# Kernel tuning notes

Hardware: AMD Instinct MI355X
Metric: run time of the kernel (lower is better)

Reference implementation:

```python
import jax, jax.numpy as jnp
import numpy as np

PAD = 20
MAX_DISP = 20
STRIDE2 = 2


def setup_inputs() -> dict:
    key = jax.random.key(0)
    k1, k2 = jax.random.split(key)
    B, C, H, W = 8, 256, 96, 128
    input1 = jax.random.normal(k1, (B, C, H, W), dtype=jnp.float32)
    input2 = jax.random.normal(k2, (B, C, H, W), dtype=jnp.float32)
    return {"input1": input1, "input2": input2}


def reference(input1, input2):
    B, C, H, W = input1.shape
    # zero-pad f2 spatially by PAD on all sides, as ZeroPad2d(pad_size)
    f2pad = jnp.pad(input2, ((0, 0), (0, 0), (PAD, PAD), (PAD, PAD)))
    # displacement offsets: range(i, i + 2*max_disp + 1, stride2) -> 21 per axis
    offs = jnp.arange(0, 2 * MAX_DISP + 1, STRIDE2)
    dy, dx = jnp.meshgrid(offs, offs, indexing="ij")  # h-major flatten matches torch flatten(-2,-1)
    dydx = jnp.stack([dy.ravel(), dx.ravel()], axis=-1)  # [441, 2]

    def step(_, d):
        # shifted view of f2pad: window element (dy, dx) for every pixel (i, j)
        win = jax.lax.dynamic_slice(f2pad, (0, 0, d[0], d[1]), (B, C, H, W))
        # per-pixel inner product over channels
        return None, jnp.einsum("bchw,bchw->bhw", input1, win)

    _, out = jax.lax.scan(step, None, dydx)  # [441, B, H, W]
    out = jnp.transpose(out, (1, 0, 2, 3))  # [B, 441, H, W]
    return out / C
```

## Files before the change

kernel.cpp:

```cpp
#include <hip/hip_runtime.h>
#include <hip/hip_bf16.h>


#define NB 8
#define NC 256
#define NH 96
#define NW 128
#define NU 64
#define ND 21
#define NK 441
#define HW (NH * NW)
#define ROWDW 8192
#define NR 97

typedef __attribute__((ext_vector_type(8))) short s16x8;
typedef __attribute__((ext_vector_type(16))) float f32x16;

__device__ __forceinline__ unsigned short f2bf(float f) {
    unsigned int x = __float_as_uint(f);
    x += 0x7fffu + ((x >> 16) & 1u);
    return (unsigned short)(x >> 16);
}

__global__ __launch_bounds__(256) void repack7(
    const float* __restrict__ in2, unsigned int* __restrict__ yg)
{
    int bid = blockIdx.x;
    int tid = threadIdx.x;

    if (bid >= NB * NH * 4) {
        int b = bid - NB * NH * 4;
        uint4 z = {0u, 0u, 0u, 0u};
        #pragma unroll
        for (int p = 0; p < 2; ++p) {
            unsigned int* base = yg + ((size_t)(b * 2 + p) * NR + 96) * ROWDW;
            #pragma unroll
            for (int m = 0; m < 8; ++m) {
                *reinterpret_cast<uint4*>(base + (m * 256 + tid) * 4) = z;
            }
        }
        return;
    }

    int ct = bid & 3;
    int rest = bid >> 2;
    int r = rest % NH;
    int b = rest / NH;
    int c0 = ct * 64;

    __shared__ unsigned short tbuf[128][68];

    int j = tid & 127;
    int ch = tid >> 7;
    #pragma unroll 4
    for (int p = 0; p < 32; ++p) {
        int cl = p * 2 + ch;
        tbuf[j][cl] = f2bf(in2[(((size_t)b * NC + (c0 + cl)) * NH + r) * NW + j]);
    }
    __syncthreads();
    int c2 = tid & 31;
    int jr = tid >> 5;
    #pragma unroll
    for (int jj0 = 0; jj0 < 128; jj0 += 8) {
        int jj = jj0 + jr;
        int pj = jj & 1, u = jj >> 1;
        unsigned int val = *reinterpret_cast<const unsigned int*>(&tbuf[jj][2 * c2]);
        size_t o = ((size_t)(b * 2 + pj) * NR + r) * ROWDW + u * 128 + ct * 32 + c2;
        yg[o] = val;
    }
}

#define GP 25
#define LDSZ (128 * GP * 4)

__global__ __launch_bounds__(512, 2) void corr7(
    const float* __restrict__ in1,
    const unsigned int* __restrict__ yg,
    float* __restrict__ out)
{
    __shared__ __align__(16) unsigned char LDS[LDSZ];

    int bid = blockIdx.x;
    int b = bid & 7;
    int i = bid >> 3;
    int tid = threadIdx.x;
    int lane = tid & 63;
    int wv = tid >> 6;
    int pj = wv >> 2;
    int ut = (wv >> 1) & 1;
    int wt = wv & 1;
    int l31 = lane & 31;
    int hp = lane >> 5;

    int ky0 = 21 - i; ky0 = (ky0 > 0) ? (ky0 >> 1) : 0;
    int ky1 = (115 - i) >> 1; if (ky1 > 20) ky1 = 20;

    int u_a = ut * 32 + l31;
    int j_a = 2 * u_a + pj;
    const float* arow = in1 + (((size_t)b * NC) * NH + i) * NW + j_a;
    s16x8 afr[16];
    #pragma unroll
    for (int ks = 0; ks < 16; ++ks) {
        int c0 = ks * 16 + hp * 8;
        s16x8 a;
        #pragma unroll
        for (int s = 0; s < 8; ++s) a[s] = (short)f2bf(arow[(size_t)(c0 + s) * HW]);
        afr[ks] = a;
    }

    int jx = tid & 127;
    int kq = tid >> 7;
    for (int ky = 0; ky < ky0; ++ky) {
        size_t ob = (((size_t)b * NK + 21 * ky) * NH + i) * NW + jx;
        for (int kx = kq; kx < ND; kx += 4) out[ob + (size_t)kx * HW] = 0.0f;
    }
    for (int ky = ky1 + 1; ky <= 20; ++ky) {
        size_t ob = (((size_t)b * NK + 21 * ky) * NH + i) * NW + jx;
        for (int kx = kq; kx < ND; kx += 4) out[ob + (size_t)kx * HW] = 0.0f;
    }

    const unsigned int* ygp = yg + (size_t)(b * 2 + pj) * NR * ROWDW;
    int w = ut * 32 - 10 + wt * 32 + l31;
    bool bval = (w >= 0) && (w < NU);
    int lane_dw = bval ? (w * 128) : 0;
    const int zrow_dw = 96 * ROWDW;

    int ue = jx >> 1, pjx = jx & 1;
    const int gebase = ((pjx * 64 + ue) * GP) * 4;

    int urow0 = pj * 64 + ut * 32;

    for (int ky = ky0; ky <= ky1; ++ky) {
        int r = i + 2 * ky - 20;
        int row_dw = bval ? (r * ROWDW) : zrow_dw;

        const s16x8* bp = reinterpret_cast<const s16x8*>(ygp + row_dw + lane_dw);
        s16x8 bfv[16];
        #pragma unroll
        for (int k8 = 0; k8 < 16; ++k8) bfv[k8] = bp[k8 * 2 + hp];

        f32x16 acc;
        #pragma unroll
        for (int z = 0; z < 16; ++z) acc[z] = 0.0f;
        #pragma unroll
        for (int k8 = 0; k8 < 16; ++k8) {
            acc = __builtin_amdgcn_mfma_f32_32x32x16_bf16(afr[k8], bfv[k8], acc, 0, 0, 0);
        }

        #pragma unroll
        for (int r16 = 0; r16 < 16; ++r16) {
            int ur = (r16 & 3) + 8 * (r16 >> 2) + 4 * hp;
            int kx = wt * 32 + l31 - ur;
            if (kx >= 0 && kx <= 20) {
                *reinterpret_cast<float*>(
                    &LDS[((urow0 + ur) * GP + kx) * 4]) = acc[r16];
            }
        }
        __syncthreads();

        size_t ob = (((size_t)b * NK + 21 * ky) * NH + i) * NW + jx;
        for (int kx = kq; kx < ND; kx += 4) {
            out[ob + (size_t)kx * HW] =
                *reinterpret_cast<const float*>(&LDS[gebase + kx * 4]) * 0.00390625f;
        }
        __syncthreads();
    }
}

__global__ __launch_bounds__(256) void corr_naive(
    const float* __restrict__ in1, const float* __restrict__ in2, float* __restrict__ out)
{
    size_t o = (size_t)blockIdx.x * 256 + threadIdx.x;
    if (o >= (size_t)NB * NK * NH * NW) return;
    int j = o & 127;
    int i = (int)((o >> 7) % NH);
    size_t rest = o / ((size_t)NH * NW);
    int k = (int)(rest % NK);
    int b = (int)(rest / NK);
    int ky = k / ND, kx = k % ND;
    int r = i + 2 * ky - 20, jc = j + 2 * kx - 20;
    float s = 0.f;
    if (r >= 0 && r < NH && jc >= 0 && jc < NW) {
        const float* p1 = in1 + (((size_t)b * NC) * NH + i) * NW + j;
        const float* p2 = in2 + (((size_t)b * NC) * NH + r) * NW + jc;
        for (int c = 0; c < NC; ++c) { s += p1[0] * p2[0]; p1 += NH * NW; p2 += NH * NW; }
    }
    out[o] = s * (1.0f / 256.0f);
}

extern "C" void kernel_launch(void* const* d_in, const int* in_sizes, int n_in,
                              void* d_out, int out_size, void* d_ws, size_t ws_size,
                              hipStream_t stream) {
    const float* in1 = (const float*)d_in[0];
    const float* in2 = (const float*)d_in[1];
    float* out = (float*)d_out;

    const size_t need = (size_t)NB * 2 * NR * ROWDW * sizeof(unsigned int);

    if (ws_size < need) {
        size_t total = (size_t)NB * NK * NH * NW;
        corr_naive<<<(int)((total + 255) / 256), 256, 0, stream>>>(in1, in2, out);
        return;
    }

    unsigned int* yg = (unsigned int*)d_ws;

    repack7<<<NB * NH * 4 + NB, 256, 0, stream>>>(in2, yg);
    corr7<<<NB * NH, 512, 0, stream>>>(in1, yg, out);
}
```

Measured before the change: 277.6 us.

## Pad repacked rows with zero slots and prefetch next B fragments during MFMA

The repack now writes each row with 10 zero slots on each side of the 64 column positions, laid out channel-group-major. This removes the per-lane validity select and the separate zero row, so corr can use a branch-free base pointer. The corr loop now loads the B fragments for the next ky row right after issuing the current MFMAs, overlapping global loads with MFMA, the LDS transpose and the output stores. The cost is a larger workspace footprint with more padding writes, plus extra registers to hold the prefetched fragments.

```diff
diff --git a/kernel.cpp b/kernel.cpp
--- a/kernel.cpp
+++ b/kernel.cpp
@@ -10,8 +10,10 @@
 #define ND 21
 #define NK 441
 #define HW (NH * NW)
-#define ROWDW 8192
-#define NR 97
+#define NSLOT 96
+#define CHDW (NSLOT * 4)
+#define ROWDW (32 * CHDW)
+#define PJDW ((size_t)NH * ROWDW)
 
 typedef __attribute__((ext_vector_type(8))) short s16x8;
 typedef __attribute__((ext_vector_type(16))) float f32x16;
@@ -22,26 +24,10 @@
     return (unsigned short)(x >> 16);
 }
 
-__global__ __launch_bounds__(256) void repack7(
+__global__ __launch_bounds__(256) void repack8(
     const float* __restrict__ in2, unsigned int* __restrict__ yg)
 {
     int bid = blockIdx.x;
-    int tid = threadIdx.x;
-
-    if (bid >= NB * NH * 4) {
-        int b = bid - NB * NH * 4;
-        uint4 z = {0u, 0u, 0u, 0u};
-        #pragma unroll
-        for (int p = 0; p < 2; ++p) {
-            unsigned int* base = yg + ((size_t)(b * 2 + p) * NR + 96) * ROWDW;
-            #pragma unroll
-            for (int m = 0; m < 8; ++m) {
-                *reinterpret_cast<uint4*>(base + (m * 256 + tid) * 4) = z;
-            }
-        }
-        return;
-    }
-
     int ct = bid & 3;
     int rest = bid >> 2;
     int r = rest % NH;
@@ -50,6 +36,7 @@
 
     __shared__ unsigned short tbuf[128][68];
 
+    int tid = threadIdx.x;
     int j = tid & 127;
     int ch = tid >> 7;
     #pragma unroll 4
@@ -58,22 +45,37 @@
         tbuf[j][cl] = f2bf(in2[(((size_t)b * NC + (c0 + cl)) * NH + r) * NW + j]);
     }
     __syncthreads();
-    int c2 = tid & 31;
-    int jr = tid >> 5;
+
     #pragma unroll
-    for (int jj0 = 0; jj0 < 128; jj0 += 8) {
-        int jj = jj0 + jr;
-        int pj = jj & 1, u = jj >> 1;
-        unsigned int val = *reinterpret_cast<const unsigned int*>(&tbuf[jj][2 * c2]);
-        size_t o = ((size_t)(b * 2 + pj) * NR + r) * ROWDW + u * 128 + ct * 32 + c2;
+    for (int it = 0; it < 16; ++it) {
+        int item = it * 256 + tid;
+        int d = item & 3;
+        int u = (item >> 2) & 63;
+        int cl8 = (item >> 8) & 7;
+        int pj = item >> 11;
+        unsigned int val = *reinterpret_cast<const unsigned int*>(&tbuf[2 * u + pj][cl8 * 8 + d * 2]);
+        size_t o = ((size_t)(b * 2 + pj) * NH + r) * ROWDW
+                 + (size_t)(ct * 8 + cl8) * CHDW + (u + 10) * 4 + d;
         yg[o] = val;
+    }
+    #pragma unroll
+    for (int it = 0; it < 8; ++it) {
+        int item = it * 256 + tid;
+        int d = item & 3;
+        int zs = (item >> 2) & 31;
+        int cl8 = (item >> 7) & 7;
+        int pj = item >> 10;
+        int slot = (zs < 10) ? zs : (zs + 64);
+        size_t o = ((size_t)(b * 2 + pj) * NH + r) * ROWDW
+                 + (size_t)(ct * 8 + cl8) * CHDW + slot * 4 + d;
+        yg[o] = 0u;
     }
 }
 
 #define GP 25
 #define LDSZ (128 * GP * 4)
 
-__global__ __launch_bounds__(512, 2) void corr7(
+__global__ __launch_bounds__(512, 2) void corr8(
     const float* __restrict__ in1,
     const unsigned int* __restrict__ yg,
     float* __restrict__ out)
@@ -95,6 +97,18 @@
     int ky0 = 21 - i; ky0 = (ky0 > 0) ? (ky0 >> 1) : 0;
     int ky1 = (115 - i) >> 1; if (ky1 > 20) ky1 = 20;
 
+    const unsigned int* lanebase = yg + (size_t)(b * 2 + pj) * PJDW
+                                 + (size_t)hp * CHDW
+                                 + (ut * 32 + wt * 32 + l31) * 4;
+
+    s16x8 bfv[16];
+    {
+        const unsigned int* p = lanebase + (size_t)(i + 2 * ky0 - 20) * ROWDW;
+        #pragma unroll
+        for (int k8 = 0; k8 < 16; ++k8)
+            bfv[k8] = *reinterpret_cast<const s16x8*>(p + (size_t)k8 * (2 * CHDW));
+    }
+
     int u_a = ut * 32 + l31;
     int j_a = 2 * u_a + pj;
     const float* arow = in1 + (((size_t)b * NC) * NH + i) * NW + j_a;
@@ -119,32 +133,25 @@
         for (int kx = kq; kx < ND; kx += 4) out[ob + (size_t)kx * HW] = 0.0f;
     }
 
-    const unsigned int* ygp = yg + (size_t)(b * 2 + pj) * NR * ROWDW;
-    int w = ut * 32 - 10 + wt * 32 + l31;
-    bool bval = (w >= 0) && (w < NU);
-    int lane_dw = bval ? (w * 128) : 0;
-    const int zrow_dw = 96 * ROWDW;
-
     int ue = jx >> 1, pjx = jx & 1;
     const int gebase = ((pjx * 64 + ue) * GP) * 4;
 
     int urow0 = pj * 64 + ut * 32;
 
     for (int ky = ky0; ky <= ky1; ++ky) {
-        int r = i + 2 * ky - 20;
-        int row_dw = bval ? (r * ROWDW) : zrow_dw;
-
-        const s16x8* bp = reinterpret_cast<const s16x8*>(ygp + row_dw + lane_dw);
-        s16x8 bfv[16];
-        #pragma unroll
-        for (int k8 = 0; k8 < 16; ++k8) bfv[k8] = bp[k8 * 2 + hp];
-
         f32x16 acc;
         #pragma unroll
         for (int z = 0; z < 16; ++z) acc[z] = 0.0f;
         #pragma unroll
         for (int k8 = 0; k8 < 16; ++k8) {
             acc = __builtin_amdgcn_mfma_f32_32x32x16_bf16(afr[k8], bfv[k8], acc, 0, 0, 0);
+        }
+
+        if (ky < ky1) {
+            const unsigned int* p = lanebase + (size_t)(i + 2 * ky - 18) * ROWDW;
+            #pragma unroll
+            for (int k8 = 0; k8 < 16; ++k8)
+                bfv[k8] = *reinterpret_cast<const s16x8*>(p + (size_t)k8 * (2 * CHDW));
         }
 
         #pragma unroll
@@ -195,7 +202,7 @@
     const float* in2 = (const float*)d_in[1];
     float* out = (float*)d_out;
 
-    const size_t need = (size_t)NB * 2 * NR * ROWDW * sizeof(unsigned int);
+    const size_t need = (size_t)NB * 2 * NH * ROWDW * sizeof(unsigned int);
 
     if (ws_size < need) {
         size_t total = (size_t)NB * NK * NH * NW;
@@ -205,6 +212,6 @@
 
     unsigned int* yg = (unsigned int*)d_ws;
 
-    repack7<<<NB * NH * 4 + NB, 256, 0, stream>>>(in2, yg);
-    corr7<<<NB * NH, 512, 0, stream>>>(in1, yg, out);
-}
+    repack8<<<NB * NH * 4, 256, 0, stream>>>(in2, yg);
+    corr8<<<NB * NH, 512, 0, stream>>>(in1, yg, out);
+}
```

Measured after the change: 236.2 us. 14.9% less time.
